# Kernel tuning notes

Measured on AMD Instinct MI355X. Metric: run time of the kernel, lower is better.

Reference implementation:

```python
import jax, jax.numpy as jnp
import numpy as np

WIN = 7
SIZE = 56
HEADS = 16
DIM = 512
SHIFT = WIN // 2  # 3


def _rel_index():
    # Matches torch.meshgrid (ij) + flatten + pairwise diff indexing of the bias table.
    coords = np.stack(np.meshgrid(np.arange(WIN), np.arange(WIN), indexing='ij')).reshape(2, -1)  # [2,49]
    rel = (coords[:, :, None] - coords[:, None, :]).transpose(1, 2, 0)  # [49,49,2]
    rel[..., 0] += WIN - 1
    rel[..., 1] += WIN - 1
    rel[..., 0] *= 2 * WIN - 1
    return (rel[..., 0] + rel[..., 1]).reshape(-1)  # [49*49]


def _attn_mask():
    # Shifted-window mask: windows mixing different regions get -100 on cross pairs.
    img = np.zeros((SIZE, SIZE))
    sl = (slice(0, -WIN), slice(-WIN, -SHIFT), slice(-SHIFT, None))
    cnt = 0
    for h in sl:
        for w in sl:
            img[h, w] = cnt
            cnt += 1
    m = img.reshape(SIZE // WIN, WIN, SIZE // WIN, WIN).transpose(0, 2, 1, 3).reshape(-1, WIN * WIN)  # [nW,49]
    am = m[:, None, :] - m[:, :, None]  # [nW,49,49]
    return np.where(am != 0, -100.0, 0.0).astype(np.float32)


_REL_IDX = _rel_index()
_MASK = _attn_mask()  # [64,49,49]


def setup_inputs() -> dict:
    key = jax.random.key(0)
    ks = jax.random.split(key, 6)
    Bn, N, C = 2048, WIN * WIN, DIM
    return {
        'x': jax.random.normal(ks[0], (Bn, N, C), jnp.float32),
        'qkv_w': jax.random.normal(ks[1], (C, 3 * C), jnp.float32) * (C ** -0.5),
        'qkv_b': jax.random.normal(ks[2], (3 * C,), jnp.float32) * 0.02,
        'proj_w': jax.random.normal(ks[3], (C, C), jnp.float32) * (C ** -0.5),
        'proj_b': jax.random.normal(ks[4], (C,), jnp.float32) * 0.02,
        'bias_table': jax.random.normal(ks[5], ((2 * WIN - 1) ** 2, HEADS), jnp.float32) * 0.02,
    }


def reference(x, qkv_w, qkv_b, proj_w, proj_b, bias_table):
    Bn, N, C = x.shape
    D = C // HEADS
    qkv = (x @ qkv_w + qkv_b).reshape(Bn, N, 3, HEADS, D).transpose(2, 0, 3, 1, 4)  # [3,Bn,H,N,D]
    q, k, v = qkv[0] * (D ** -0.5), qkv[1], qkv[2]
    attn = jnp.einsum('bhnd,bhmd->bhnm', q, k)  # [Bn,H,N,N]
    bias = bias_table[jnp.asarray(_REL_IDX)].reshape(N, N, HEADS).transpose(2, 0, 1)  # [H,N,N]
    attn = attn + bias[None]
    mask = jnp.asarray(_MASK, x.dtype)  # [nW,N,N]
    nW = mask.shape[0]
    attn = attn.reshape(Bn // nW, nW, HEADS, N, N) + mask[None, :, None]
    attn = jax.nn.softmax(attn.reshape(Bn, HEADS, N, N), axis=-1)
    out = jnp.einsum('bhnm,bhmd->bhnd', attn, v).transpose(0, 2, 1, 3).reshape(Bn, N, C)
    return out @ proj_w + proj_b
```

## Files before the change

kernel.cpp:

```cpp
#include <hip/hip_runtime.h>
#include <hip/hip_bf16.h>
#include <stdint.h>


#define HEADS 16
#define NTOK  49
#define CH    512

typedef float  f32x4  __attribute__((ext_vector_type(4)));
typedef __bf16 bf16x8 __attribute__((ext_vector_type(8)));
typedef unsigned short u16;
typedef unsigned int   u32;

__device__ __forceinline__ u16 f2bf(float f) {
  return __builtin_bit_cast(u16, (__bf16)f);
}

__device__ __forceinline__ void gload16(const u16* g, u16* l) {
  __builtin_amdgcn_global_load_lds(
      (const __attribute__((address_space(1))) u32*)g,
      (__attribute__((address_space(3))) u32*)l, 16, 0, 0);
}

__global__ __launch_bounds__(256) void k_wprep(const float* __restrict__ qkv_w,
                                               const float* __restrict__ proj_w,
                                               const float* __restrict__ qkv_b,
                                               u16* __restrict__ Wt, u16* __restrict__ Pt,
                                               float* __restrict__ bias2) {
  const float sc = 0.17677669529663687f;
  int tid = blockIdx.x * 256 + threadIdx.x;
  const int T1 = 1536 * 512;
  if (tid < 1536) bias2[tid] = qkv_b[tid] * (tid < 512 ? sc : 1.f);
  if (tid < T1) {
    int n = tid >> 9, k = tid & 511;
    float v = qkv_w[k * 1536 + n];
    if (n < 512) v *= sc;
    Wt[tid] = f2bf(v);
  } else {
    int t2 = tid - T1;
    int n = t2 >> 9, k = t2 & 511;
    Pt[t2] = f2bf(proj_w[k * 512 + n]);
  }
}

__global__ __launch_bounds__(256) void k_xcast(const float* __restrict__ x,
                                               u16* __restrict__ xb) {
  int tid = blockIdx.x * 256 + threadIdx.x;
  const float4* xv = (const float4*)x;
  float4 a = xv[tid * 2], b = xv[tid * 2 + 1];
  u16 o[8] = {f2bf(a.x), f2bf(a.y), f2bf(a.z), f2bf(a.w),
              f2bf(b.x), f2bf(b.y), f2bf(b.z), f2bf(b.w)};
  ((int4*)xb)[tid] = *(const int4*)o;
}

__global__ __launch_bounds__(256) void k_tabs(const float* __restrict__ bias_table,
                                              float* __restrict__ biasM,
                                              float* __restrict__ maskT) {
  int tid = blockIdx.x * 256 + threadIdx.x;
  if (tid < 16 * 4096) {
    int h = tid >> 12, rc = tid & 4095, r = rc >> 6, c = rc & 63;
    float v = -1e30f;
    if (r < NTOK && c < NTOK) {
      int ih = r / 7, iw = r - ih * 7, jh = c / 7, jw = c - jh * 7;
      v = bias_table[((ih - jh + 6) * 13 + (iw - jw + 6)) * HEADS + h];
    }
    biasM[tid] = v;
  } else {
    int t2 = tid - 65536;
    int mw = t2 >> 12, rc = t2 & 4095, r = rc >> 6, c = rc & 63;
    float v = 0.f;
    if (r < NTOK && c < NTOK) {
      int mwR = (mw >> 3) * 7, mwC = (mw & 7) * 7;
      int ih = r / 7, iw = r - ih * 7, jh = c / 7, jw = c - jh * 7;
      int gih = mwR + ih, giw = mwC + iw, gjh = mwR + jh, gjw = mwC + jw;
      int ri = (gih < 49 ? 0 : (gih < 53 ? 1 : 2)) * 3 + (giw < 49 ? 0 : (giw < 53 ? 1 : 2));
      int rj = (gjh < 49 ? 0 : (gjh < 53 ? 1 : 2)) * 3 + (gjw < 49 ? 0 : (gjw < 53 ? 1 : 2));
      v = (ri != rj) ? -100.f : 0.f;
    }
    maskT[t2] = v;
  }
}

template<int OUT_F32>
__global__ __launch_bounds__(256) void k_gemm(const u16* __restrict__ A,
                                              const u16* __restrict__ Bt,
                                              const float* __restrict__ bias,
                                              void* __restrict__ Cp,
                                              int M, int Nn, int K, int nbn) {
  __shared__ u16 smem[128 * 136];
  u16* sA = smem;
  u16* sB = smem + 8192;
  const int t   = threadIdx.x;
  const int bid = blockIdx.x;
  const int cb  = bid % nbn, rb = bid / nbn;
  const int row0 = rb << 7, col0 = cb << 7;
  const int lane = t & 63, w = t >> 6;
  const int wr = (w >> 1) << 6, wc = (w & 1) << 6;
  const int lm = lane & 15, lk = lane >> 4;

  const f32x4 fz = {0.f, 0.f, 0.f, 0.f};
  f32x4 acc[4][4];
#pragma unroll
  for (int i = 0; i < 4; i++)
#pragma unroll
    for (int j = 0; j < 4; j++) acc[i][j] = fz;

  int gr[4], gc[4], gdb[4];
#pragma unroll
  for (int i = 0; i < 4; ++i) {
    int q = (i << 8) + t;
    gr[i]  = q >> 3;
    gc[i]  = (((q & 7) ^ (gr[i] & 7)) << 3);
    gdb[i] = ((i << 8) + (t & 192)) << 3;
  }
  int offA[4], offB[4];
#pragma unroll
  for (int i = 0; i < 4; ++i) {
    int rowA = wr + i * 16 + lm;
    offA[i] = rowA * 64 + ((lk ^ (rowA & 7)) << 3);
    int rowB = wc + i * 16 + lm;
    offB[i] = rowB * 64 + ((lk ^ (rowB & 7)) << 3);
  }

  const int nk = K >> 6;
  for (int kt = 0; kt < nk; ++kt) {
    const int kb = kt << 6;
    __syncthreads();
#pragma unroll
    for (int i = 0; i < 4; ++i) {
      gload16(A  + (size_t)(row0 + gr[i]) * K + kb + gc[i], sA + gdb[i]);
      gload16(Bt + (size_t)(col0 + gr[i]) * K + kb + gc[i], sB + gdb[i]);
    }
    __syncthreads();
    bf16x8 a[4][2], b[4][2];
#pragma unroll
    for (int mi = 0; mi < 4; ++mi) {
      a[mi][0] = *(const bf16x8*)(sA + offA[mi]);
      a[mi][1] = *(const bf16x8*)(sA + (offA[mi] ^ 32));
    }
#pragma unroll
    for (int ni = 0; ni < 4; ++ni) {
      b[ni][0] = *(const bf16x8*)(sB + offB[ni]);
      b[ni][1] = *(const bf16x8*)(sB + (offB[ni] ^ 32));
    }
#pragma unroll
    for (int kk = 0; kk < 2; ++kk)
#pragma unroll
      for (int mi = 0; mi < 4; ++mi)
#pragma unroll
        for (int ni = 0; ni < 4; ++ni)
          acc[mi][ni] = __builtin_amdgcn_mfma_f32_16x16x32_bf16(a[mi][kk], b[ni][kk],
                                                                acc[mi][ni], 0, 0, 0);
  }

  if constexpr (!OUT_F32) {
    __syncthreads();
#pragma unroll
    for (int mi = 0; mi < 4; ++mi)
#pragma unroll
      for (int ni = 0; ni < 4; ++ni) {
        int col = wc + ni * 16 + lm;
        float bv = bias[col0 + col];
#pragma unroll
        for (int r = 0; r < 4; ++r)
          smem[(wr + mi * 16 + lk * 4 + r) * 136 + col] = f2bf(acc[mi][ni][r] + bv);
      }
    __syncthreads();
    const int rr = t >> 1, seg = t & 1;
    u16* dst = (u16*)Cp + (size_t)(row0 + rr) * Nn + col0 + seg * 64;
    const u16* src = smem + rr * 136 + seg * 64;
#pragma unroll
    for (int i = 0; i < 8; ++i)
      *(int4*)(dst + i * 8) = *(const int4*)(src + i * 8);
  } else {
    float* smf = (float*)smem;
    for (int half = 0; half < 2; ++half) {
      __syncthreads();
      if ((w >> 1) == half) {
#pragma unroll
        for (int mi = 0; mi < 4; ++mi)
#pragma unroll
          for (int ni = 0; ni < 4; ++ni) {
            int col = wc + ni * 16 + lm;
            float bv = bias[col0 + col];
#pragma unroll
            for (int r = 0; r < 4; ++r)
              smf[(mi * 16 + lk * 4 + r) * 132 + col] = acc[mi][ni][r] + bv;
          }
      }
      __syncthreads();
      const int rr = t >> 2, seg = t & 3;
      float* dst = (float*)Cp + (size_t)(row0 + half * 64 + rr) * Nn + col0 + seg * 32;
      const float* src = smf + rr * 132 + seg * 32;
#pragma unroll
      for (int i = 0; i < 8; ++i)
        *(float4*)(dst + i * 4) = *(const float4*)(src + i * 4);
    }
  }
}

__global__ __launch_bounds__(256) void k_attn(const u16* __restrict__ qkv,
                                              const float* __restrict__ biasM,
                                              const float* __restrict__ maskT,
                                              u16* __restrict__ aout) {
  __shared__ u16 sm[4 * 6528];
  const int bid = blockIdx.x;
  const int wdx = bid >> 2;
  const int wv  = threadIdx.x >> 6;
  const int h   = ((bid & 3) << 2) + wv;
  const int mw  = wdx & 63;
  const int l   = threadIdx.x & 63;
  const int lm  = l & 15, lk = l >> 4;
  const size_t tb = (size_t)wdx * NTOK;
  const u16* base = qkv + tb * 1536;
  u16* sP = sm + wv * 6528;
  u16* sV = sP + 4352;

  const int4  iz = make_int4(0, 0, 0, 0);
  const f32x4 fz = {0.f, 0.f, 0.f, 0.f};

  {
    const int n = l;
    const u16* vp = base + (size_t)n * 1536 + 1024 + h * 32;
#pragma unroll
    for (int d0 = 0; d0 < 4; d0++) {
      int4 vv = (n < NTOK) ? *(const int4*)(vp + d0 * 8) : iz;
      const u16* u = (const u16*)&vv;
#pragma unroll
      for (int j = 0; j < 8; j++) sV[(d0 * 8 + j) * 68 + n] = u[j];
    }
  }

  bf16x8 qf[4], kf[4];
#pragma unroll
  for (int i = 0; i < 4; i++) {
    int m = i * 16 + lm;
    int4 qi = (m < NTOK) ? *(const int4*)(base + (size_t)m * 1536 +       h * 32 + lk * 8) : iz;
    int4 ki = (m < NTOK) ? *(const int4*)(base + (size_t)m * 1536 + 512 + h * 32 + lk * 8) : iz;
    qf[i] = __builtin_bit_cast(bf16x8, qi);
    kf[i] = __builtin_bit_cast(bf16x8, ki);
  }

  f32x4 s[4][4];
#pragma unroll
  for (int mi = 0; mi < 4; mi++)
#pragma unroll
    for (int ni = 0; ni < 4; ni++)
      s[mi][ni] = __builtin_amdgcn_mfma_f32_16x16x32_bf16(qf[mi], kf[ni], fz, 0, 0, 0);

  const float* bM = biasM + (h << 12);
  const float* mT = maskT + (mw << 12);
  float rinv[4][4];

#pragma unroll
  for (int mi = 0; mi < 4; mi++) {
    float rmax[4] = {-3e38f, -3e38f, -3e38f, -3e38f};
#pragma unroll
    for (int ni = 0; ni < 4; ni++) {
#pragma unroll
      for (int r = 0; r < 4; r++) {
        int off = mi * 1024 + lk * 256 + r * 64 + ni * 16 + lm;
        float v = s[mi][ni][r] + bM[off] + mT[off];
        s[mi][ni][r] = v;
        rmax[r] = fmaxf(rmax[r], v);
      }
    }
#pragma unroll
    for (int r = 0; r < 4; r++) {
      float m = rmax[r];
#pragma unroll
      for (int d = 1; d < 16; d <<= 1) m = fmaxf(m, __shfl_xor(m, d, 64));
      rmax[r] = m;
    }
    float rsum[4] = {0.f, 0.f, 0.f, 0.f};
#pragma unroll
    for (int ni = 0; ni < 4; ni++) {
#pragma unroll
      for (int r = 0; r < 4; r++) {
        float p = __expf(s[mi][ni][r] - rmax[r]);
        s[mi][ni][r] = p;
        rsum[r] += p;
      }
    }
#pragma unroll
    for (int r = 0; r < 4; r++) {
      float sm2 = rsum[r];
#pragma unroll
      for (int d = 1; d < 16; d <<= 1) sm2 += __shfl_xor(sm2, d, 64);
      rinv[mi][r] = 1.f / sm2;
    }
#pragma unroll
    for (int ni = 0; ni < 4; ni++)
#pragma unroll
      for (int r = 0; r < 4; r++)
        sP[(mi * 16 + lk * 4 + r) * 68 + ni * 16 + lm] = f2bf(s[mi][ni][r]);
  }

  f32x4 o[4][2];
#pragma unroll
  for (int mi = 0; mi < 4; mi++) { o[mi][0] = fz; o[mi][1] = fz; }
#pragma unroll
  for (int kt = 0; kt < 2; kt++) {
    bf16x8 vb[2];
#pragma unroll
    for (int df = 0; df < 2; df++)
      vb[df] = *(const bf16x8*)(sV + (df * 16 + lm) * 68 + kt * 32 + lk * 8);
#pragma unroll
    for (int mi = 0; mi < 4; mi++) {
      bf16x8 pa = *(const bf16x8*)(sP + (mi * 16 + lm) * 68 + kt * 32 + lk * 8);
      o[mi][0] = __builtin_amdgcn_mfma_f32_16x16x32_bf16(pa, vb[0], o[mi][0], 0, 0, 0);
      o[mi][1] = __builtin_amdgcn_mfma_f32_16x16x32_bf16(pa, vb[1], o[mi][1], 0, 0, 0);
    }
  }

#pragma unroll
  for (int mi = 0; mi < 4; mi++) {
#pragma unroll
    for (int r = 0; r < 4; r++) {
      int row = mi * 16 + lk * 4 + r;
      if (row < NTOK) {
        float inv = rinv[mi][r];
        size_t ob = (tb + row) * CH + h * 32;
        aout[ob + lm]      = f2bf(o[mi][0][r] * inv);
        aout[ob + 16 + lm] = f2bf(o[mi][1][r] * inv);
      }
    }
  }
}

extern "C" void kernel_launch(void* const* d_in, const int* in_sizes, int n_in,
                              void* d_out, int out_size, void* d_ws, size_t ws_size,
                              hipStream_t stream) {
  const float* x      = (const float*)d_in[0];
  const float* qkv_b  = (const float*)d_in[2];
  const float* proj_b = (const float*)d_in[4];
  const float* btab   = (const float*)d_in[5];

  char* ws   = (char*)d_ws;
  u16* Wt    = (u16*)ws;
  u16* Pt    = (u16*)(ws + 1572864);
  u16* qkv   = (u16*)(ws + 2097152);
  u16* aout  = (u16*)(ws + 2097152 + 308281344ull);
  u16* xb    = aout;
  float* biasM = (float*)(ws + 2097152 + 308281344ull + 102760448ull);
  float* maskT = biasM + 65536;
  float* bias2 = maskT + 262144;
  float* out = (float*)d_out;

  k_wprep<<<4096, 256, 0, stream>>>((const float*)d_in[1], (const float*)d_in[3],
                                    qkv_b, Wt, Pt, bias2);
  k_xcast<<<25088, 256, 0, stream>>>(x, xb);
  k_tabs<<<1280, 256, 0, stream>>>(btab, biasM, maskT);
  k_gemm<0><<<784 * 12, 256, 0, stream>>>(xb, Wt, bias2, (void*)qkv, 100352, 1536, 512, 12);
  k_attn<<<2048 * 4, 256, 0, stream>>>(qkv, biasM, maskT, aout);
  k_gemm<1><<<784 * 4, 256, 0, stream>>>(aout, Pt, proj_b, (void*)out, 100352, 512, 512, 4);
}
```

Baseline: 733.2 us.

## Split attention work so each wave handles one 16-row query tile per head

The attention kernel now assigns one (window, head) pair per block, with each of its four waves computing one 16-query-row tile. Previously a single wave handled all 64 rows of one head. Scores are computed transposed (K×Q), so each lane's softmax row reduction needs only two cross-lane shuffles, and the normalized probabilities are packed into LDS with 8-byte stores. V is cooperatively loaded once per block and shared across waves, which requires a block barrier. This cuts per-wave register pressure and increases grid parallelism fourfold, at the cost of reloading K and bias/mask rows per wave and launching more blocks.

```diff
diff --git a/kernel.cpp b/kernel.cpp
--- a/kernel.cpp
+++ b/kernel.cpp
@@ -203,127 +203,107 @@
                                               const float* __restrict__ biasM,
                                               const float* __restrict__ maskT,
                                               u16* __restrict__ aout) {
-  __shared__ u16 sm[4 * 6528];
+  __shared__ u16 sV[32 * 68];
+  __shared__ u16 sP[4 * 16 * 68];
   const int bid = blockIdx.x;
-  const int wdx = bid >> 2;
-  const int wv  = threadIdx.x >> 6;
-  const int h   = ((bid & 3) << 2) + wv;
+  const int wdx = bid >> 4;
+  const int h   = bid & 15;
   const int mw  = wdx & 63;
-  const int l   = threadIdx.x & 63;
+  const int t   = threadIdx.x;
+  const int wv  = t >> 6;
+  const int l   = t & 63;
   const int lm  = l & 15, lk = l >> 4;
   const size_t tb = (size_t)wdx * NTOK;
   const u16* base = qkv + tb * 1536;
-  u16* sP = sm + wv * 6528;
-  u16* sV = sP + 4352;
 
   const int4  iz = make_int4(0, 0, 0, 0);
   const f32x4 fz = {0.f, 0.f, 0.f, 0.f};
 
   {
-    const int n = l;
-    const u16* vp = base + (size_t)n * 1536 + 1024 + h * 32;
-#pragma unroll
-    for (int d0 = 0; d0 < 4; d0++) {
-      int4 vv = (n < NTOK) ? *(const int4*)(vp + d0 * 8) : iz;
+    if (l < NTOK) {
+      int4 vv = *(const int4*)(base + (size_t)l * 1536 + 1024 + h * 32 + wv * 8);
       const u16* u = (const u16*)&vv;
 #pragma unroll
-      for (int j = 0; j < 8; j++) sV[(d0 * 8 + j) * 68 + n] = u[j];
-    }
-  }
-
-  bf16x8 qf[4], kf[4];
-#pragma unroll
-  for (int i = 0; i < 4; i++) {
-    int m = i * 16 + lm;
-    int4 qi = (m < NTOK) ? *(const int4*)(base + (size_t)m * 1536 +       h * 32 + lk * 8) : iz;
-    int4 ki = (m < NTOK) ? *(const int4*)(base + (size_t)m * 1536 + 512 + h * 32 + lk * 8) : iz;
-    qf[i] = __builtin_bit_cast(bf16x8, qi);
-    kf[i] = __builtin_bit_cast(bf16x8, ki);
-  }
-
-  f32x4 s[4][4];
-#pragma unroll
-  for (int mi = 0; mi < 4; mi++)
-#pragma unroll
-    for (int ni = 0; ni < 4; ni++)
-      s[mi][ni] = __builtin_amdgcn_mfma_f32_16x16x32_bf16(qf[mi], kf[ni], fz, 0, 0, 0);
-
-  const float* bM = biasM + (h << 12);
-  const float* mT = maskT + (mw << 12);
-  float rinv[4][4];
-
-#pragma unroll
-  for (int mi = 0; mi < 4; mi++) {
-    float rmax[4] = {-3e38f, -3e38f, -3e38f, -3e38f};
-#pragma unroll
-    for (int ni = 0; ni < 4; ni++) {
-#pragma unroll
-      for (int r = 0; r < 4; r++) {
-        int off = mi * 1024 + lk * 256 + r * 64 + ni * 16 + lm;
-        float v = s[mi][ni][r] + bM[off] + mT[off];
-        s[mi][ni][r] = v;
-        rmax[r] = fmaxf(rmax[r], v);
-      }
-    }
+      for (int j = 0; j < 8; j++) sV[(wv * 8 + j) * 68 + l] = u[j];
+    } else {
+#pragma unroll
+      for (int j = 0; j < 8; j++) sV[(wv * 8 + j) * 68 + l] = 0;
+    }
+  }
+
+  const int qrow = wv * 16 + lm;
+  int4 qi = (qrow < NTOK) ? *(const int4*)(base + (size_t)qrow * 1536 + h * 32 + lk * 8) : iz;
+  bf16x8 qf = __builtin_bit_cast(bf16x8, qi);
+  bf16x8 kf[4];
+#pragma unroll
+  for (int ni = 0; ni < 4; ni++) {
+    int krow = ni * 16 + lm;
+    int4 ki = (krow < NTOK) ? *(const int4*)(base + (size_t)krow * 1536 + 512 + h * 32 + lk * 8) : iz;
+    kf[ni] = __builtin_bit_cast(bf16x8, ki);
+  }
+
+  f32x4 st[4];
+#pragma unroll
+  for (int ni = 0; ni < 4; ni++)
+    st[ni] = __builtin_amdgcn_mfma_f32_16x16x32_bf16(kf[ni], qf, fz, 0, 0, 0);
+
+  const float* bM = biasM + (h << 12) + (qrow << 6);
+  const float* mT = maskT + (mw << 12) + (qrow << 6);
+  float mx = -3e38f;
+#pragma unroll
+  for (int ni = 0; ni < 4; ni++) {
 #pragma unroll
     for (int r = 0; r < 4; r++) {
-      float m = rmax[r];
-#pragma unroll
-      for (int d = 1; d < 16; d <<= 1) m = fmaxf(m, __shfl_xor(m, d, 64));
-      rmax[r] = m;
-    }
-    float rsum[4] = {0.f, 0.f, 0.f, 0.f};
-#pragma unroll
-    for (int ni = 0; ni < 4; ni++) {
-#pragma unroll
-      for (int r = 0; r < 4; r++) {
-        float p = __expf(s[mi][ni][r] - rmax[r]);
-        s[mi][ni][r] = p;
-        rsum[r] += p;
-      }
-    }
+      int kk = ni * 16 + lk * 4 + r;
+      float v = st[ni][r] + bM[kk] + mT[kk];
+      st[ni][r] = v;
+      mx = fmaxf(mx, v);
+    }
+  }
+  mx = fmaxf(mx, __shfl_xor(mx, 16, 64));
+  mx = fmaxf(mx, __shfl_xor(mx, 32, 64));
+  float sum = 0.f;
+#pragma unroll
+  for (int ni = 0; ni < 4; ni++) {
 #pragma unroll
     for (int r = 0; r < 4; r++) {
-      float sm2 = rsum[r];
-#pragma unroll
-      for (int d = 1; d < 16; d <<= 1) sm2 += __shfl_xor(sm2, d, 64);
-      rinv[mi][r] = 1.f / sm2;
-    }
-#pragma unroll
-    for (int ni = 0; ni < 4; ni++)
-#pragma unroll
-      for (int r = 0; r < 4; r++)
-        sP[(mi * 16 + lk * 4 + r) * 68 + ni * 16 + lm] = f2bf(s[mi][ni][r]);
-  }
-
-  f32x4 o[4][2];
-#pragma unroll
-  for (int mi = 0; mi < 4; mi++) { o[mi][0] = fz; o[mi][1] = fz; }
+      float p = __expf(st[ni][r] - mx);
+      st[ni][r] = p;
+      sum += p;
+    }
+  }
+  sum += __shfl_xor(sum, 16, 64);
+  sum += __shfl_xor(sum, 32, 64);
+  const float rinv = 1.f / sum;
+
+  u16* sPw = sP + wv * (16 * 68);
+#pragma unroll
+  for (int ni = 0; ni < 4; ni++) {
+    u16 pk[4] = {f2bf(st[ni][0] * rinv), f2bf(st[ni][1] * rinv),
+                 f2bf(st[ni][2] * rinv), f2bf(st[ni][3] * rinv)};
+    *(int2*)(sPw + lm * 68 + ni * 16 + lk * 4) = *(const int2*)pk;
+  }
+
+  __syncthreads();
+
+  f32x4 o[2] = {fz, fz};
 #pragma unroll
   for (int kt = 0; kt < 2; kt++) {
-    bf16x8 vb[2];
-#pragma unroll
-    for (int df = 0; df < 2; df++)
-      vb[df] = *(const bf16x8*)(sV + (df * 16 + lm) * 68 + kt * 32 + lk * 8);
-#pragma unroll
-    for (int mi = 0; mi < 4; mi++) {
-      bf16x8 pa = *(const bf16x8*)(sP + (mi * 16 + lm) * 68 + kt * 32 + lk * 8);
-      o[mi][0] = __builtin_amdgcn_mfma_f32_16x16x32_bf16(pa, vb[0], o[mi][0], 0, 0, 0);
-      o[mi][1] = __builtin_amdgcn_mfma_f32_16x16x32_bf16(pa, vb[1], o[mi][1], 0, 0, 0);
-    }
-  }
-
-#pragma unroll
-  for (int mi = 0; mi < 4; mi++) {
-#pragma unroll
-    for (int r = 0; r < 4; r++) {
-      int row = mi * 16 + lk * 4 + r;
-      if (row < NTOK) {
-        float inv = rinv[mi][r];
-        size_t ob = (tb + row) * CH + h * 32;
-        aout[ob + lm]      = f2bf(o[mi][0][r] * inv);
-        aout[ob + 16 + lm] = f2bf(o[mi][1][r] * inv);
-      }
+    bf16x8 pa = *(const bf16x8*)(sPw + lm * 68 + kt * 32 + lk * 8);
+#pragma unroll
+    for (int df = 0; df < 2; df++) {
+      bf16x8 vb = *(const bf16x8*)(sV + (df * 16 + lm) * 68 + kt * 32 + lk * 8);
+      o[df] = __builtin_amdgcn_mfma_f32_16x16x32_bf16(pa, vb, o[df], 0, 0, 0);
+    }
+  }
+
+#pragma unroll
+  for (int r = 0; r < 4; r++) {
+    int tok = wv * 16 + lk * 4 + r;
+    if (tok < NTOK) {
+      size_t ob = (tb + tok) * CH + h * 32;
+      aout[ob + lm]      = f2bf(o[0][r]);
+      aout[ob + 16 + lm] = f2bf(o[1][r]);
     }
   }
 }
@@ -352,6 +332,6 @@
   k_xcast<<<25088, 256, 0, stream>>>(x, xb);
   k_tabs<<<1280, 256, 0, stream>>>(btab, biasM, maskT);
   k_gemm<0><<<784 * 12, 256, 0, stream>>>(xb, Wt, bias2, (void*)qkv, 100352, 1536, 512, 12);
-  k_attn<<<2048 * 4, 256, 0, stream>>>(qkv, biasM, maskT, aout);
+  k_attn<<<2048 * 16, 256, 0, stream>>>(qkv, biasM, maskT, aout);
   k_gemm<1><<<784 * 4, 256, 0, stream>>>(aout, Pt, proj_b, (void*)out, 100352, 512, 512, 4);
 }
```

Result: slower. 809.2 us (+10.4%).
